# Kernel optimization log

Measured on AMD Instinct MI355X. Metric: run time of the kernel, lower is better.

## Reference

```python
import jax, jax.numpy as jnp
import numpy as np

NUM_CAPSULE = 10
DIM_CAPSULE = 16
ROUTINGS = 3
EPS = 1e-7  # K.epsilon()


def squash(x, axis=-1):
    sq_norm = jnp.sum(jnp.square(x), axis=axis, keepdims=True) + EPS
    coeff = jnp.sqrt(sq_norm) / (1.0 + sq_norm)
    return coeff * x


def setup_inputs() -> dict:
    key = jax.random.key(0)
    k1, k2 = jax.random.split(key)
    B, I, Din = 64, 4096, 128
    u_vecs = jax.random.normal(k1, (B, I, Din), dtype=jnp.float32)
    # glorot-ish scale for the capsule kernel (flattened conv1d kernel of size 1)
    W = jax.random.normal(k2, (Din, NUM_CAPSULE * DIM_CAPSULE), dtype=jnp.float32) * 0.06
    return {"u_vecs": u_vecs, "W": W}


def reference(u_vecs, W):
    B, I, Din = u_vecs.shape
    N, D = NUM_CAPSULE, DIM_CAPSULE
    # conv1d with kernel size 1 == per-position matmul
    u_hat = jnp.einsum('bid,dk->bik', u_vecs, W)          # [B, I, N*D]
    u_hat = u_hat.reshape(B, I, N, D).transpose(0, 2, 1, 3)  # [B, N, I, D]

    b = jnp.zeros((B, N, I), dtype=u_hat.dtype)
    outputs = None
    for i in range(ROUTINGS):
        c = jax.nn.softmax(b, axis=1)                      # softmax over num_capsule
        s = jnp.einsum('bni,bnid->bnd', c, u_hat)          # weighted sum over input caps
        outputs = squash(s)                                # [B, N, D]
        if i < ROUTINGS - 1:
            b = jnp.einsum('bnd,bnid->bni', outputs, u_hat)  # agreement logits
    return outputs
```

## Files before the change

### kernel.cpp

```cpp
#include <hip/hip_runtime.h>
#include <hip/hip_bf16.h>
#include <math.h>

#define NCAP 10
#define DCAP 16
#define DIN  128
#define NPOS 4096
#define NB   64

typedef short short8 __attribute__((ext_vector_type(8)));
typedef float floatx4 __attribute__((ext_vector_type(4)));

__device__ inline float bflo(unsigned v) { return __uint_as_float(v << 16); }
__device__ inline float bfhi(unsigned v) { return __uint_as_float(v & 0xFFFF0000u); }
__device__ inline unsigned short f2bf(float f) {
    unsigned u = __float_as_uint(f);
    return (unsigned short)((u + 0x7FFFu + ((u >> 16) & 1u)) >> 16);
}
__device__ inline float bf2f(unsigned short h) { return __uint_as_float(((unsigned)h) << 16); }


__global__ __launch_bounds__(256) void wprep(const float* __restrict__ W,
                                             uint4* __restrict__ WTg) {
    const int cid = blockIdx.x * 256 + threadIdx.x;
    if (cid >= 2560) return;
    const int row = cid >> 4;
    const int csn = cid & 15;
    const int kc = csn ^ (row & 15);
    unsigned p[4];
    #pragma unroll
    for (int e = 0; e < 4; ++e) {
        const float a = W[(kc * 8 + e * 2) * 160 + row];
        const float b = W[(kc * 8 + e * 2 + 1) * 160 + row];
        p[e] = (unsigned)f2bf(a) | ((unsigned)f2bf(b) << 16);
    }
    WTg[cid] = make_uint4(p[0], p[1], p[2], p[3]);
}

__global__ __launch_bounds__(256, 3) void gemm_uhat(const float* __restrict__ u,
                                                    const uint4* __restrict__ WTg,
                                                    uint4* __restrict__ uhat4,
                                                    float* __restrict__ partial) {
    const int b = blockIdx.x;
    const int blk = blockIdx.y;
    const int t = threadIdx.x;
    const int l = t & 63;
    const int wv = __builtin_amdgcn_readfirstlane(t >> 6);

    __shared__ __align__(16) char lds[40960 + 11264];
    uint4* WT4 = (uint4*)lds;
    short* out16 = (short*)(lds + 40960);
    float* csbuf = (float*)(lds + 40960);

    #pragma unroll
    for (int i = 0; i < 10; ++i)
        WT4[t + i * 256] = WTg[t + i * 256];
    __syncthreads();

    float cs[4][8];
    #pragma unroll
    for (int kk = 0; kk < 4; ++kk)
        #pragma unroll
        for (int e = 0; e < 8; ++e) cs[kk][e] = 0.f;

    const short8* wt8 = (const short8*)lds;
    const float4* u4g = (const float4*)u;

    for (int mt = 0; mt < 4; ++mt) {
        const size_t row = (size_t)b * NPOS + blk * 256 + mt * 64 + wv * 16 + (l & 15);
        short8 af[4];
        #pragma unroll
        for (int kk = 0; kk < 4; ++kk) {
            const float4 x0 = u4g[row * 32 + kk * 8 + (l >> 4) * 2];
            const float4 x1 = u4g[row * 32 + kk * 8 + (l >> 4) * 2 + 1];
            cs[kk][0] += x0.x; cs[kk][1] += x0.y; cs[kk][2] += x0.z; cs[kk][3] += x0.w;
            cs[kk][4] += x1.x; cs[kk][5] += x1.y; cs[kk][6] += x1.z; cs[kk][7] += x1.w;
            short8 a;
            a[0] = (short)f2bf(x0.x); a[1] = (short)f2bf(x0.y);
            a[2] = (short)f2bf(x0.z); a[3] = (short)f2bf(x0.w);
            a[4] = (short)f2bf(x1.x); a[5] = (short)f2bf(x1.y);
            a[6] = (short)f2bf(x1.z); a[7] = (short)f2bf(x1.w);
            af[kk] = a;
        }

        floatx4 acc[10];
        #pragma unroll
        for (int n = 0; n < 10; ++n) {
            floatx4 a = {0.f, 0.f, 0.f, 0.f};
            #pragma unroll
            for (int kk = 0; kk < 4; ++kk) {
                const short8 bf = wt8[(n * 16 + (l & 15)) * 16 +
                                      ((kk * 4 + (l >> 4)) ^ (l & 15))];
                a = __builtin_amdgcn_mfma_f32_16x16x32_bf16(af[kk], bf, a, 0, 0, 0);
            }
            acc[n] = a;
        }

        #pragma unroll
        for (int h = 0; h < 2; ++h) {
            __syncthreads();
            if ((wv >> 1) == h) {
                const int r0 = (wv & 1) * 16 + (l >> 4) * 4;
                #pragma unroll
                for (int n = 0; n < 10; ++n)
                    #pragma unroll
                    for (int reg = 0; reg < 4; ++reg)
                        out16[(r0 + reg) * 176 + n * 16 + (l & 15)] =
                            (short)f2bf(acc[n][reg]);
            }
            __syncthreads();
            const uint4* o4 = (const uint4*)out16;
            const size_t gb = ((size_t)b * NPOS + blk * 256 + mt * 64 + h * 32) * 20;
            #pragma unroll
            for (int i = 0; i < 3; ++i) {
                const int q = t + i * 256;
                if (q < 640)
                    uhat4[gb + q] = o4[(q / 20) * 22 + (q % 20)];
            }
        }
    }

    __syncthreads();
    #pragma unroll
    for (int kk = 0; kk < 4; ++kk)
        #pragma unroll
        for (int e = 0; e < 8; ++e) {
            float v = cs[kk][e];
            v += __shfl_xor(v, 1); v += __shfl_xor(v, 2);
            v += __shfl_xor(v, 4); v += __shfl_xor(v, 8);
            cs[kk][e] = v;
        }
    if ((l & 15) == 0) {
        #pragma unroll
        for (int kk = 0; kk < 4; ++kk)
            #pragma unroll
            for (int e = 0; e < 8; ++e)
                csbuf[wv * 128 + kk * 32 + (l >> 4) * 8 + e] = cs[kk][e];
    }
    __syncthreads();
    if (t < 128)
        partial[(size_t)(b * 16 + blk) * 128 + t] =
            csbuf[t] + csbuf[128 + t] + csbuf[256 + t] + csbuf[384 + t];
}

__global__ __launch_bounds__(128) void small0(const float* __restrict__ partial,
                                              const float* __restrict__ W,
                                              float* __restrict__ vbuf) {
    const int b = blockIdx.x / NCAP;
    const int n = blockIdx.x % NCAP;
    const int t = threadIdx.x;
    __shared__ float xv[DIN];
    float a = 0.f;
    #pragma unroll 4
    for (int c = 0; c < 16; ++c)
        a += partial[(size_t)(b * 16 + c) * DIN + t];
    xv[t] = a;
    __syncthreads();
    if (t < DCAP) {
        float sv = 0.f;
        for (int d = 0; d < DIN; ++d)
            sv = fmaf(xv[d], W[d * 160 + n * DCAP + t], sv);
        sv *= 0.1f;
        float nq = sv * sv;
        #pragma unroll
        for (int mm = 8; mm >= 1; mm >>= 1) nq += __shfl_xor(nq, mm, 16);
        nq += 1e-7f;
        vbuf[(size_t)(b * NCAP + n) * DCAP + t] = sv * sqrtf(nq) / (1.0f + nq);
    }
}

__global__ __launch_bounds__(256, 4) void route_uhat(const uint4* __restrict__ uhat4,
                                                     const float* __restrict__ vbuf,
                                                     float* __restrict__ pws) {
    const int b = blockIdx.x;
    const int blk = blockIdx.y;
    const int t = threadIdx.x;
    const int l = t & 63;
    const int wv = __builtin_amdgcn_readfirstlane(t >> 6);

    __shared__ __align__(16) char tl[64 * 336];
    __shared__ float lgp[4][64][10];
    __shared__ float cs[64][10];
    short* tls = (short*)tl;
    uint4* tl4 = (uint4*)tl;

    const float* vb = vbuf + (size_t)b * 160;
    float acc = 0.f;

    for (int s = 0; s < 4; ++s) {
        __syncthreads();
        const size_t base4 = ((size_t)b * NPOS + blk * 256 + s * 64) * 20;
        #pragma unroll
        for (int i = 0; i < 5; ++i) {
            const int q = t + i * 256;
            tl4[(q / 20) * 21 + (q % 20)] = uhat4[base4 + q];
        }
        __syncthreads();

        float lg[10];
        #pragma unroll
        for (int n = 0; n < 10; ++n) {
            const uint2 uu = *(const uint2*)&tls[l * 168 + n * 16 + wv * 4];
            lg[n] = bflo(uu.x) * vb[n * 16 + wv * 4]
                  + bfhi(uu.x) * vb[n * 16 + wv * 4 + 1]
                  + bflo(uu.y) * vb[n * 16 + wv * 4 + 2]
                  + bfhi(uu.y) * vb[n * 16 + wv * 4 + 3];
            lgp[wv][l][n] = lg[n];
        }
        __syncthreads();

        float c[10];
        float m = -1e30f;
        #pragma unroll
        for (int n = 0; n < 10; ++n) {
            c[n] = lgp[0][l][n] + lgp[1][l][n] + lgp[2][l][n] + lgp[3][l][n];
            m = fmaxf(m, c[n]);
        }
        float ssum = 0.f;
        #pragma unroll
        for (int n = 0; n < 10; ++n) { c[n] = __expf(c[n] - m); ssum += c[n]; }
        const float inv = 1.0f / ssum;
        if (wv == 0) {
            #pragma unroll
            for (int n = 0; n < 10; ++n) cs[l][n] = c[n] * inv;
        }
        __syncthreads();

        if (t < 160) {
            const int n = t >> 4;
            for (int p = 0; p < 64; ++p)
                acc = fmaf(cs[p][n], bf2f((unsigned short)tls[p * 168 + t]), acc);
        }
    }
    if (t < 160) pws[(size_t)(b * 16 + blk) * 160 + t] = acc;
}

__global__ __launch_bounds__(256) void smallv(const float* __restrict__ pws,
                                              float* __restrict__ dst) {
    const int b = blockIdx.x;
    const int t = threadIdx.x;
    if (t >= 160) return;
    float a = 0.f;
    #pragma unroll
    for (int c = 0; c < 16; ++c)
        a += pws[(size_t)(b * 16 + c) * 160 + t];
    float nq = a * a;
    #pragma unroll
    for (int mm = 8; mm >= 1; mm >>= 1) nq += __shfl_xor(nq, mm, 16);
    nq += 1e-7f;
    dst[(size_t)b * 160 + t] = a * sqrtf(nq) / (1.0f + nq);
}


__global__ __launch_bounds__(256) void caps_sum(const float* __restrict__ u,
                                                float* __restrict__ partial) {
    const int b = blockIdx.x;
    const int chunk = blockIdx.y;
    const int t = threadIdx.x;
    const int v4 = t & 31;
    const int prow = t >> 5;
    const float4* up = (const float4*)u;
    const size_t posbase = (size_t)b * NPOS + chunk * 256;
    float4 acc = make_float4(0.f, 0.f, 0.f, 0.f);
    #pragma unroll 8
    for (int j = 0; j < 32; ++j) {
        float4 x = up[(posbase + prow + j * 8) * 32 + v4];
        acc.x += x.x; acc.y += x.y; acc.z += x.z; acc.w += x.w;
    }
    __shared__ float4 red[8][32];
    red[prow][v4] = acc;
    __syncthreads();
    if (t < 32) {
        float4 s = red[0][t];
        #pragma unroll
        for (int r = 1; r < 8; ++r) {
            s.x += red[r][t].x; s.y += red[r][t].y;
            s.z += red[r][t].z; s.w += red[r][t].w;
        }
        ((float4*)partial)[((size_t)b * 16 + chunk) * 32 + t] = s;
    }
}

template <int MODE>
__global__ __launch_bounds__(128) void caps_small(const float* __restrict__ src,
                                                  const float* __restrict__ W,
                                                  float* __restrict__ dst) {
    const int b = blockIdx.x / NCAP;
    const int n = blockIdx.x % NCAP;
    const int t = threadIdx.x;
    __shared__ float xv[DIN];
    __shared__ float vv[DCAP];
    float a = 0.f;
    if (MODE == 0) {
        #pragma unroll 4
        for (int c = 0; c < 16; ++c) a += src[(size_t)(b * 16 + c) * DIN + t];
    } else {
        #pragma unroll 4
        for (int c = 0; c < 16; ++c) a += src[((size_t)(b * 16 + c) * NCAP + n) * DIN + t];
    }
    xv[t] = a;
    __syncthreads();
    if (t < DCAP) {
        float sv = 0.f;
        for (int d = 0; d < DIN; ++d) sv = fmaf(xv[d], W[d * 160 + n * DCAP + t], sv);
        if (MODE == 0) sv *= 0.1f;
        float nq = sv * sv;
        #pragma unroll
        for (int mm = 8; mm >= 1; mm >>= 1) nq += __shfl_xor(nq, mm, 16);
        nq += 1e-7f;
        const float v = sv * sqrtf(nq) / (1.0f + nq);
        if (MODE == 2) dst[(size_t)(b * NCAP + n) * DCAP + t] = v;
        else vv[t] = v;
    }
    if (MODE != 2) {
        __syncthreads();
        float wd = 0.f;
        #pragma unroll
        for (int dd = 0; dd < DCAP; ++dd)
            wd = fmaf(W[t * 160 + n * DCAP + dd], vv[dd], wd);
        dst[(size_t)(b * NCAP + n) * DIN + t] = wd;
    }
}

__global__ __launch_bounds__(256, 3) void caps_route(const float* __restrict__ u,
                                                     const float* __restrict__ wsrc,
                                                     float* __restrict__ pdst) {
    const int b = blockIdx.x;
    const int tile = blockIdx.y;
    const int t = threadIdx.x;
    const int lane = t & 63;
    const int wv = __builtin_amdgcn_readfirstlane(t >> 6);
    __shared__ float4 tl4[64 * 32];
    __shared__ float lgp[4][64][11];
    float* tlf = (float*)tl4;
    const float4* wq4 = (const float4*)(wsrc + (size_t)b * (NCAP * DIN));
    float acc0[NCAP], acc1[NCAP];
    #pragma unroll
    for (int n = 0; n < NCAP; ++n) { acc0[n] = 0.f; acc1[n] = 0.f; }
    for (int s = 0; s < 4; ++s) {
        __syncthreads();
        const float4* src4 = (const float4*)u + ((size_t)b * NPOS + tile * 256 + s * 64) * 32;
        #pragma unroll
        for (int i = 0; i < 8; ++i) {
            const int q = t + i * 256;
            const int r = q >> 5, c = q & 31;
            tl4[r * 32 + (c ^ (r & 7))] = src4[q];
        }
        __syncthreads();
        float lg[NCAP];
        #pragma unroll
        for (int n = 0; n < NCAP; ++n) lg[n] = 0.f;
        #pragma unroll
        for (int j = 0; j < 8; ++j) {
            const float4 u4 = tl4[lane * 32 + wv * 8 + (j ^ (lane & 7))];
            #pragma unroll
            for (int n = 0; n < NCAP; ++n) {
                const float4 w4 = wq4[n * 32 + wv * 8 + j];
                lg[n] = fmaf(u4.x, w4.x, fmaf(u4.y, w4.y,
                        fmaf(u4.z, w4.z, fmaf(u4.w, w4.w, lg[n]))));
            }
        }
        #pragma unroll
        for (int n = 0; n < NCAP; ++n) lgp[wv][lane][n] = lg[n];
        __syncthreads();
        float c[NCAP];
        float m = -1e30f;
        #pragma unroll
        for (int n = 0; n < NCAP; ++n) {
            c[n] = lgp[0][lane][n] + lgp[1][lane][n] + lgp[2][lane][n] + lgp[3][lane][n];
            m = fmaxf(m, c[n]);
        }
        float ssum = 0.f;
        #pragma unroll
        for (int n = 0; n < NCAP; ++n) { c[n] = __expf(c[n] - m); ssum += c[n]; }
        const float inv = 1.0f / ssum;
        #pragma unroll
        for (int n = 0; n < NCAP; ++n) c[n] *= inv;
        const int col0 = lane >> 2, word = lane & 3;
        #pragma unroll
        for (int i = 0; i < 16; ++i) {
            const int p = wv * 16 + i;
            const int ca = col0 ^ (p & 7);
            const float u0 = tlf[(p * 32 + ca) * 4 + word];
            const float u1 = tlf[(p * 32 + ca + 16) * 4 + word];
            #pragma unroll
            for (int n = 0; n < NCAP; ++n) {
                const float cp = __int_as_float(
                    __builtin_amdgcn_readlane(__float_as_int(c[n]), p));
                acc0[n] = fmaf(cp, u0, acc0[n]);
                acc1[n] = fmaf(cp, u1, acc1[n]);
            }
        }
    }
    __syncthreads();
    float* red = tlf;
    #pragma unroll
    for (int n = 0; n < NCAP; ++n) {
        red[(wv * NCAP + n) * DIN + lane]      = acc0[n];
        red[(wv * NCAP + n) * DIN + lane + 64] = acc1[n];
    }
    __syncthreads();
    float* pb = pdst + (size_t)(b * 16 + tile) * (NCAP * DIN);
    for (int k = t; k < NCAP * DIN; k += 256)
        pb[k] = red[k] + red[1280 + k] + red[2560 + k] + red[3840 + k];
}

extern "C" void kernel_launch(void* const* d_in, const int* in_sizes, int n_in,
                              void* d_out, int out_size, void* d_ws, size_t ws_size,
                              hipStream_t stream) {
    const float* u = (const float*)d_in[0];
    const float* W = (const float*)d_in[1];
    float* out = (float*)d_out;
    char* wsb = (char*)d_ws;

    if (ws_size >= 85147648ull) {
        float* partial = (float*)wsb;
        float* vbuf    = (float*)(wsb + 524288);
        float* pws     = (float*)(wsb + 565248);
        uint4* WTg     = (uint4*)(wsb + 1220608);
        uint4* uhat    = (uint4*)(wsb + 1261568);

        wprep<<<10, 256, 0, stream>>>(W, WTg);
        gemm_uhat<<<dim3(NB, 16), 256, 0, stream>>>(u, WTg, uhat, partial);
        small0<<<NB * NCAP, 128, 0, stream>>>(partial, W, vbuf);
        route_uhat<<<dim3(NB, 16), 256, 0, stream>>>(uhat, vbuf, pws);
        smallv<<<NB, 256, 0, stream>>>(pws, vbuf);
        route_uhat<<<dim3(NB, 16), 256, 0, stream>>>(uhat, vbuf, pws);
        smallv<<<NB, 256, 0, stream>>>(pws, out);
    } else {
        float* partial = (float*)wsb;
        float* wbuf    = (float*)wsb + 131072;
        float* pws32   = (float*)wsb + 212992;
        caps_sum<<<dim3(NB, 16), 256, 0, stream>>>(u, partial);
        caps_small<0><<<NB * NCAP, 128, 0, stream>>>(partial, W, wbuf);
        caps_route<<<dim3(NB, 16), 256, 0, stream>>>(u, wbuf, pws32);
        caps_small<1><<<NB * NCAP, 128, 0, stream>>>(pws32, W, wbuf);
        caps_route<<<dim3(NB, 16), 256, 0, stream>>>(u, wbuf, pws32);
        caps_small<2><<<NB * NCAP, 128, 0, stream>>>(pws32, W, out);
    }
}
```

Baseline: 111.2 us.

## Store u_hat in MFMA fragment layout and route directly from registers

The GEMM now swaps MFMA operands and writes each u_hat accumulator fragment straight to global memory in its native register layout. This removes the LDS transpose staging and its barriers. The routing kernel reads these fragments directly, computes logits and softmax with cross-lane shuffles, and reduces the weighted sums in registers. That drops the LDS tile copies and several syncthreads, and it runs on a 4x larger grid. The cost is 4x more partial sums for the smallv reduction, plus 8-byte global stores instead of 16-byte coalesced stores.

Result: slower. 133.2 us (+19.8%).

```diff
diff --git a/kernel.cpp b/kernel.cpp
--- a/kernel.cpp
+++ b/kernel.cpp
@@ -17,7 +17,6 @@
     unsigned u = __float_as_uint(f);
     return (unsigned short)((u + 0x7FFFu + ((u >> 16) & 1u)) >> 16);
 }
-__device__ inline float bf2f(unsigned short h) { return __uint_as_float(((unsigned)h) << 16); }
 
 
 __global__ __launch_bounds__(256) void wprep(const float* __restrict__ W,
@@ -37,20 +36,17 @@
     WTg[cid] = make_uint4(p[0], p[1], p[2], p[3]);
 }
 
-__global__ __launch_bounds__(256, 3) void gemm_uhat(const float* __restrict__ u,
-                                                    const uint4* __restrict__ WTg,
-                                                    uint4* __restrict__ uhat4,
-                                                    float* __restrict__ partial) {
+__global__ __launch_bounds__(256) void gemm_uhat(const float* __restrict__ u,
+                                                 const uint4* __restrict__ WTg,
+                                                 uint2* __restrict__ uf2,
+                                                 float* __restrict__ partial) {
     const int b = blockIdx.x;
     const int blk = blockIdx.y;
     const int t = threadIdx.x;
     const int l = t & 63;
     const int wv = __builtin_amdgcn_readfirstlane(t >> 6);
 
-    __shared__ __align__(16) char lds[40960 + 11264];
-    uint4* WT4 = (uint4*)lds;
-    short* out16 = (short*)(lds + 40960);
-    float* csbuf = (float*)(lds + 40960);
+    __shared__ uint4 WT4[2560];
 
     #pragma unroll
     for (int i = 0; i < 10; ++i)
@@ -63,12 +59,13 @@
         #pragma unroll
         for (int e = 0; e < 8; ++e) cs[kk][e] = 0.f;
 
-    const short8* wt8 = (const short8*)lds;
+    const short8* wt8 = (const short8*)WT4;
     const float4* u4g = (const float4*)u;
 
+    #pragma unroll 1
     for (int mt = 0; mt < 4; ++mt) {
         const size_t row = (size_t)b * NPOS + blk * 256 + mt * 64 + wv * 16 + (l & 15);
-        short8 af[4];
+        short8 bfr[4];
         #pragma unroll
         for (int kk = 0; kk < 4; ++kk) {
             const float4 x0 = u4g[row * 32 + kk * 8 + (l >> 4) * 2];
@@ -80,47 +77,28 @@
             a[2] = (short)f2bf(x0.z); a[3] = (short)f2bf(x0.w);
             a[4] = (short)f2bf(x1.x); a[5] = (short)f2bf(x1.y);
             a[6] = (short)f2bf(x1.z); a[7] = (short)f2bf(x1.w);
-            af[kk] = a;
-        }
-
-        floatx4 acc[10];
-        #pragma unroll
+            bfr[kk] = a;
+        }
+
+        const size_t cell = (((size_t)(b * 16 + blk) * 4 + mt) * 4 + wv) * 10;
+        #pragma unroll 2
         for (int n = 0; n < 10; ++n) {
             floatx4 a = {0.f, 0.f, 0.f, 0.f};
             #pragma unroll
             for (int kk = 0; kk < 4; ++kk) {
-                const short8 bf = wt8[(n * 16 + (l & 15)) * 16 +
+                const short8 wf = wt8[(n * 16 + (l & 15)) * 16 +
                                       ((kk * 4 + (l >> 4)) ^ (l & 15))];
-                a = __builtin_amdgcn_mfma_f32_16x16x32_bf16(af[kk], bf, a, 0, 0, 0);
+                a = __builtin_amdgcn_mfma_f32_16x16x32_bf16(wf, bfr[kk], a, 0, 0, 0);
             }
-            acc[n] = a;
-        }
-
-        #pragma unroll
-        for (int h = 0; h < 2; ++h) {
-            __syncthreads();
-            if ((wv >> 1) == h) {
-                const int r0 = (wv & 1) * 16 + (l >> 4) * 4;
-                #pragma unroll
-                for (int n = 0; n < 10; ++n)
-                    #pragma unroll
-                    for (int reg = 0; reg < 4; ++reg)
-                        out16[(r0 + reg) * 176 + n * 16 + (l & 15)] =
-                            (short)f2bf(acc[n][reg]);
-            }
-            __syncthreads();
-            const uint4* o4 = (const uint4*)out16;
-            const size_t gb = ((size_t)b * NPOS + blk * 256 + mt * 64 + h * 32) * 20;
-            #pragma unroll
-            for (int i = 0; i < 3; ++i) {
-                const int q = t + i * 256;
-                if (q < 640)
-                    uhat4[gb + q] = o4[(q / 20) * 22 + (q % 20)];
-            }
-        }
-    }
-
-    __syncthreads();
+            uint2 pk;
+            pk.x = (unsigned)f2bf(a[0]) | ((unsigned)f2bf(a[1]) << 16);
+            pk.y = (unsigned)f2bf(a[2]) | ((unsigned)f2bf(a[3]) << 16);
+            uf2[(cell + n) * 64 + l] = pk;
+        }
+    }
+
+    __syncthreads();
+    float* csbuf = (float*)WT4;
     #pragma unroll
     for (int kk = 0; kk < 4; ++kk)
         #pragma unroll
@@ -169,70 +147,71 @@
     }
 }
 
-__global__ __launch_bounds__(256, 4) void route_uhat(const uint4* __restrict__ uhat4,
-                                                     const float* __restrict__ vbuf,
-                                                     float* __restrict__ pws) {
+__global__ __launch_bounds__(256) void route_uf(const uint2* __restrict__ uf2,
+                                                const float* __restrict__ vbuf,
+                                                float* __restrict__ pws) {
     const int b = blockIdx.x;
-    const int blk = blockIdx.y;
+    const int g = blockIdx.y;
     const int t = threadIdx.x;
     const int l = t & 63;
-    const int wv = __builtin_amdgcn_readfirstlane(t >> 6);
-
-    __shared__ __align__(16) char tl[64 * 336];
-    __shared__ float lgp[4][64][10];
-    __shared__ float cs[64][10];
-    short* tls = (short*)tl;
-    uint4* tl4 = (uint4*)tl;
-
-    const float* vb = vbuf + (size_t)b * 160;
-    float acc = 0.f;
-
-    for (int s = 0; s < 4; ++s) {
-        __syncthreads();
-        const size_t base4 = ((size_t)b * NPOS + blk * 256 + s * 64) * 20;
-        #pragma unroll
-        for (int i = 0; i < 5; ++i) {
-            const int q = t + i * 256;
-            tl4[(q / 20) * 21 + (q % 20)] = uhat4[base4 + q];
-        }
-        __syncthreads();
-
-        float lg[10];
-        #pragma unroll
-        for (int n = 0; n < 10; ++n) {
-            const uint2 uu = *(const uint2*)&tls[l * 168 + n * 16 + wv * 4];
-            lg[n] = bflo(uu.x) * vb[n * 16 + wv * 4]
-                  + bfhi(uu.x) * vb[n * 16 + wv * 4 + 1]
-                  + bflo(uu.y) * vb[n * 16 + wv * 4 + 2]
-                  + bfhi(uu.y) * vb[n * 16 + wv * 4 + 3];
-            lgp[wv][l][n] = lg[n];
-        }
-        __syncthreads();
-
-        float c[10];
-        float m = -1e30f;
-        #pragma unroll
-        for (int n = 0; n < 10; ++n) {
-            c[n] = lgp[0][l][n] + lgp[1][l][n] + lgp[2][l][n] + lgp[3][l][n];
-            m = fmaxf(m, c[n]);
-        }
-        float ssum = 0.f;
-        #pragma unroll
-        for (int n = 0; n < 10; ++n) { c[n] = __expf(c[n] - m); ssum += c[n]; }
-        const float inv = 1.0f / ssum;
-        if (wv == 0) {
+    const int w = __builtin_amdgcn_readfirstlane(t >> 6);
+
+    const size_t cell = (((size_t)(b * 16 + (g >> 2)) * 4 + (g & 3)) * 4 + w) * 10;
+
+    float vals[10][4];
+    float lg[10];
+    #pragma unroll
+    for (int n = 0; n < 10; ++n) {
+        const uint2 q = uf2[(cell + n) * 64 + l];
+        vals[n][0] = bflo(q.x); vals[n][1] = bfhi(q.x);
+        vals[n][2] = bflo(q.y); vals[n][3] = bfhi(q.y);
+        const float4 vq = *(const float4*)&vbuf[(size_t)(b * 10 + n) * 16 + (l >> 4) * 4];
+        lg[n] = vals[n][0] * vq.x + vals[n][1] * vq.y +
+                vals[n][2] * vq.z + vals[n][3] * vq.w;
+    }
+    #pragma unroll
+    for (int n = 0; n < 10; ++n) {
+        lg[n] += __shfl_xor(lg[n], 16);
+        lg[n] += __shfl_xor(lg[n], 32);
+    }
+    float m = lg[0];
+    #pragma unroll
+    for (int n = 1; n < 10; ++n) m = fmaxf(m, lg[n]);
+    float ssum = 0.f;
+    float c[10];
+    #pragma unroll
+    for (int n = 0; n < 10; ++n) { c[n] = __expf(lg[n] - m); ssum += c[n]; }
+    const float inv = 1.0f / ssum;
+
+    float sp[10][4];
+    #pragma unroll
+    for (int n = 0; n < 10; ++n) {
+        const float cn = c[n] * inv;
+        #pragma unroll
+        for (int r = 0; r < 4; ++r) sp[n][r] = cn * vals[n][r];
+    }
+    #pragma unroll
+    for (int n = 0; n < 10; ++n)
+        #pragma unroll
+        for (int r = 0; r < 4; ++r) {
+            float v = sp[n][r];
+            v += __shfl_xor(v, 1); v += __shfl_xor(v, 2);
+            v += __shfl_xor(v, 4); v += __shfl_xor(v, 8);
+            sp[n][r] = v;
+        }
+
+    __shared__ float sm[4][160];
+    if ((l & 15) == 0) {
+        #pragma unroll
+        for (int n = 0; n < 10; ++n)
             #pragma unroll
-            for (int n = 0; n < 10; ++n) cs[l][n] = c[n] * inv;
-        }
-        __syncthreads();
-
-        if (t < 160) {
-            const int n = t >> 4;
-            for (int p = 0; p < 64; ++p)
-                acc = fmaf(cs[p][n], bf2f((unsigned short)tls[p * 168 + t]), acc);
-        }
-    }
-    if (t < 160) pws[(size_t)(b * 16 + blk) * 160 + t] = acc;
+            for (int r = 0; r < 4; ++r)
+                sm[w][n * 16 + (l >> 4) * 4 + r] = sp[n][r];
+    }
+    __syncthreads();
+    if (t < 160)
+        pws[(size_t)(b * 64 + g) * 160 + t] =
+            sm[0][t] + sm[1][t] + sm[2][t] + sm[3][t];
 }
 
 __global__ __launch_bounds__(256) void smallv(const float* __restrict__ pws,
@@ -241,9 +220,9 @@
     const int t = threadIdx.x;
     if (t >= 160) return;
     float a = 0.f;
-    #pragma unroll
-    for (int c = 0; c < 16; ++c)
-        a += pws[(size_t)(b * 16 + c) * 160 + t];
+    #pragma unroll 8
+    for (int c = 0; c < 64; ++c)
+        a += pws[(size_t)(b * 64 + c) * 160 + t];
     float nq = a * a;
     #pragma unroll
     for (int mm = 8; mm >= 1; mm >>= 1) nq += __shfl_xor(nq, mm, 16);
@@ -413,19 +392,19 @@
     float* out = (float*)d_out;
     char* wsb = (char*)d_ws;
 
-    if (ws_size >= 85147648ull) {
+    if (ws_size >= 86679552ull) {
         float* partial = (float*)wsb;
-        float* vbuf    = (float*)(wsb + 524288);
-        float* pws     = (float*)(wsb + 565248);
-        uint4* WTg     = (uint4*)(wsb + 1220608);
-        uint4* uhat    = (uint4*)(wsb + 1261568);
+        float* pws     = (float*)wsb;
+        float* vbuf    = (float*)(wsb + 2621440);
+        uint4* WTg     = (uint4*)(wsb + 2662400);
+        uint2* uf2     = (uint2*)(wsb + 2703360);
 
         wprep<<<10, 256, 0, stream>>>(W, WTg);
-        gemm_uhat<<<dim3(NB, 16), 256, 0, stream>>>(u, WTg, uhat, partial);
+        gemm_uhat<<<dim3(NB, 16), 256, 0, stream>>>(u, WTg, uf2, partial);
         small0<<<NB * NCAP, 128, 0, stream>>>(partial, W, vbuf);
-        route_uhat<<<dim3(NB, 16), 256, 0, stream>>>(uhat, vbuf, pws);
+        route_uf<<<dim3(NB, 64), 256, 0, stream>>>(uf2, vbuf, pws);
         smallv<<<NB, 256, 0, stream>>>(pws, vbuf);
-        route_uhat<<<dim3(NB, 16), 256, 0, stream>>>(uhat, vbuf, pws);
+        route_uf<<<dim3(NB, 64), 256, 0, stream>>>(uf2, vbuf, pws);
         smallv<<<NB, 256, 0, stream>>>(pws, out);
     } else {
         float* partial = (float*)wsb;
```
